# Performance work log

Hardware: AMD Instinct MI355X
Metric: run time of the kernel (lower is better)

The kernel has to match this reference:

```python
import jax, jax.numpy as jnp
import numpy as np

N_S, N_G, D, K = 30000, 3000, 128, 16
SIGMA = 2.5
BOX = 60.0  # Angstrom box for random coordinates


def setup_inputs() -> dict:
    key = jax.random.key(0)
    ks = jax.random.split(key, 10)
    s = 1.0 / np.sqrt(D)
    return {
        'xs': jax.random.normal(ks[0], (N_S, D), jnp.float32),
        'xg': jax.random.normal(ks[1], (N_G, D), jnp.float32),
        'pos_s': jax.random.uniform(ks[2], (N_S, 3), jnp.float32) * BOX,
        'pos_g': jax.random.uniform(ks[3], (N_G, 3), jnp.float32) * BOX,
        'W_s_pre': jax.random.normal(ks[4], (D, D), jnp.float32) * s,
        'W_g_pre': jax.random.normal(ks[5], (D, D), jnp.float32) * s,
        'W_gs': jax.random.normal(ks[6], (D, D), jnp.float32) * s,
        'W_sg': jax.random.normal(ks[7], (D, D), jnp.float32) * s,
        'W_s_post': jax.random.normal(ks[8], (2 * D, D), jnp.float32) * s,
        'W_g_post': jax.random.normal(ks[9], (2 * D, D), jnp.float32) * s,
        'k': K,
    }


def reference(xs, xg, pos_s, pos_g, W_s_pre, W_g_pre, W_gs, W_sg, W_s_post, W_g_post, k):
    n_s, d = xs.shape
    # ---- compute_bipartite_graphs: knn of each graph node over surface nodes ----
    # squared pairwise distances via gemm form: (N_G, N_S)
    d2 = ((pos_g ** 2).sum(-1)[:, None] + (pos_s ** 2).sum(-1)[None, :]
          - 2.0 * pos_g @ pos_s.T)
    neg_d2, idx = jax.lax.top_k(-d2, k)          # idx: (N_G, K) surface neighbors
    w = jnp.exp(neg_d2 / (2.0 * SIGMA ** 2))     # RBF edge weight exp(-d^2/(2*sigma^2))
    # ---- pre blocks ----
    hs = xs @ W_s_pre                             # (N_S, D)
    hg = xg @ W_g_pre                             # (N_G, D)
    # ---- bp_gs block: graph -> surface weighted edge-conv (scatter-add) ----
    msg_gs = (hg @ W_gs)[:, None, :] * w[:, :, None]          # (N_G, K, D)
    xs_out = jnp.zeros((n_s, d), hs.dtype).at[idx.reshape(-1)].add(
        msg_gs.reshape(-1, d))
    # ---- bp_sg block: surface -> graph weighted edge-conv (gather-sum) ----
    xg_out = ((hs @ W_sg)[idx] * w[:, :, None]).sum(axis=1)   # (N_G, D)
    # ---- post blocks: combine pre features with message output ----
    xs_new = jax.nn.relu(jnp.concatenate([hs, xs_out], axis=-1) @ W_s_post)
    xg_new = jax.nn.relu(jnp.concatenate([hg, xg_out], axis=-1) @ W_g_post)
    return xs_new, xg_new
```

## Files before the change

kernel.cpp:

```cpp
#include <hip/hip_runtime.h>
#include <stdint.h>

#define N_S 30000
#define N_G 3000
#define DD  128
#define KK  16
#define NE  (N_G * KK)
#define NC  16
#define CELLS (NC * NC * NC)
#define CH  3.75f
#define CAP 16
#define SURV 384
#define ECAP 32
#define EOVF_CAP 8192

#define FILL_BLOCKS 118
#define PACK_BLOCKS 384
#define NBS16 1875
#define NBG16 188
#define PRE_TILES (NBS16 + NBG16)
#define GROUPS 1032
#define GRID3 (GROUPS * 5)
#define NBS 469
#define NBG 47
#define NTILE (NBS + NBG)

typedef unsigned long long ull;
#define INF_KEY 0x7F7FFFFF7FFFFFFFull

using v8s = __attribute__((ext_vector_type(8))) short;
using v4f = __attribute__((ext_vector_type(4))) float;

__device__ __forceinline__ float bf2f(unsigned short u) {
    union { unsigned int i; float f; } v; v.i = ((unsigned int)u) << 16; return v.f;
}
__device__ __forceinline__ unsigned short f2bf(float f) {
    union { float f; unsigned int i; } v; v.f = f;
    unsigned int x = v.i;
    return (unsigned short)((x + 0x7fffu + ((x >> 16) & 1u)) >> 16);
}
__device__ __forceinline__ float ldIn(const void* p, int i, int bf) {
    return bf ? bf2f(((const unsigned short*)p)[i]) : ((const float*)p)[i];
}
__device__ __forceinline__ void stOut(void* p, int i, float v, int bf) {
    if (bf) ((unsigned short*)p)[i] = f2bf(v);
    else    ((float*)p)[i] = v;
}
__device__ __forceinline__ int cellOf(float x) {
    int c = (int)(x * (1.0f / CH));
    if (c < 0) c = 0; if (c > NC - 1) c = NC - 1;
    return c;
}
__device__ __forceinline__ float dist2(float gx, float gy, float gz, float4 cd) {
    const float dx = gx - cd.x, dy = gy - cd.y, dz = gz - cd.z;
    return fmaf(dx, dx, fmaf(dy, dy, dz * dz));
}
__device__ __forceinline__ ull packKey(float d2, int sid) {
    return ((ull)__float_as_uint(d2) << 32) | (unsigned)sid;
}

__device__ __forceinline__ int detectFlag(const void* pos_g) {
    const unsigned int* w = (const unsigned int*)pos_g;
    int votes = 0;
#pragma unroll
    for (int i = 0; i < 16; ++i) {
        const unsigned int b = (w[i] >> 8) & 0xFFu;
        votes += (b >= 0x3Eu && b <= 0x42u) ? 1 : 0;
    }
    return votes >= 8;
}

__device__ __forceinline__ void emitEdge(int g, ull key, int rank,
                                         int* __restrict__ idx_out,
                                         float* __restrict__ w_out,
                                         int* __restrict__ scnt,
                                         int2* __restrict__ edge,
                                         int4* __restrict__ eovf,
                                         int* __restrict__ neovf)
{
    const int sid = (int)(unsigned)key;
    const float d2 = __uint_as_float((unsigned)(key >> 32));
    const float wv = expf(-d2 * (1.0f / 12.5f));
    idx_out[g * KK + rank] = sid;
    w_out[g * KK + rank] = wv;
    const int c = atomicAdd(&scnt[sid], 1);
    if (c < ECAP) {
        edge[(size_t)sid * ECAP + c] = make_int2(g, __float_as_int(wv));
    } else {
        const int o = atomicAdd(neovf, 1);
        if (o < EOVF_CAP) eovf[o] = make_int4(sid, g, __float_as_int(wv), 0);
    }
}

__device__ __forceinline__ void ins16(ull key, ull bk[KK]) {
    if (key >= bk[KK - 1]) return;
    ull c = key;
#pragma unroll
    for (int j = 0; j < KK; ++j) {
        const bool less = c < bk[j];
        const ull nk = less ? c : bk[j];
        const ull ok = less ? bk[j] : c;
        bk[j] = nk; c = ok;
    }
}

template<int R>
__device__ __forceinline__ float regionM2f(float gx, float gy, float gz,
                                           int cx, int cy, int cz)
{
    float m = 1e30f;
    if (cx - R > 0)      m = fminf(m, gx - (float)(cx - R) * CH);
    if (cx + R < NC - 1) m = fminf(m, (float)(cx + R + 1) * CH - gx);
    if (cy - R > 0)      m = fminf(m, gy - (float)(cy - R) * CH);
    if (cy + R < NC - 1) m = fminf(m, (float)(cy + R + 1) * CH - gy);
    if (cz - R > 0)      m = fminf(m, gz - (float)(cz - R) * CH);
    if (cz + R < NC - 1) m = fminf(m, (float)(cz + R + 1) * CH - gz);
    m = fmaxf(m, 0.f);
    return (m < 1e29f) ? m * m * (1.0f - 1e-5f) : 1e30f;
}

template<int R>
__device__ int scanR(int t, float gx, float gy, float gz,
                     int cx, int cy, int cz, float m2eff,
                     const int* __restrict__ ccnt,
                     const float4* __restrict__ scell,
                     const float4* __restrict__ ovf, int novf,
                     ull* __restrict__ skey)
{
    const int S = 2 * R + 1;
    const int S3 = S * S * S;
    int total = 0;

    for (int b0 = 0; b0 < 2 * S3; b0 += 64) {
        const int pt = b0 + t;
        int cnt = 0, base = 0;
        if (pt < 2 * S3) {
            const int cell = pt >> 1, h = pt & 1;
            const int dx = cell / (S * S) - R;
            const int dy = (cell / S) % S - R;
            const int dz = cell % S - R;
            const int X = cx + dx, Y = cy + dy, Z = cz + dz;
            if (X >= 0 && X < NC && Y >= 0 && Y < NC && Z >= 0 && Z < NC) {
                const int cid = (X * NC + Y) * NC + Z;
                int c = ccnt[cid]; if (c > CAP) c = CAP;
                const int lo = h * 8;
                const int hi = (c < lo + 8) ? c : (lo + 8);
                cnt = (hi > lo) ? (hi - lo) : 0;
                base = cid * CAP + lo;
            }
        }
        ull kv[8]; int okm = 0;
#pragma unroll
        for (int i = 0; i < 8; ++i) {
            kv[i] = 0;
            if (i < cnt) {
                const float4 cd = scell[base + i];
                const float d2 = dist2(gx, gy, gz, cd);
                if (d2 < m2eff) { okm |= (1 << i); kv[i] = packKey(d2, __float_as_int(cd.w)); }
            }
        }
        int myc = __popc(okm);
        int incl = myc;
        for (int d = 1; d < 64; d <<= 1) {
            int v = __shfl_up(incl, d);
            if (t >= d) incl += v;
        }
        int pos = total + (incl - myc);
        total += __shfl(incl, 63);
#pragma unroll
        for (int i = 0; i < 8; ++i) {
            if (okm & (1 << i)) {
                if (pos < SURV) skey[pos] = kv[i];
                ++pos;
            }
        }
        if (total > SURV) return total;
    }

    for (int i0 = 0; i0 < novf; i0 += 64) {
        const int i = i0 + t;
        bool act = (i < novf);
        ull key = 0;
        if (act) {
            const float4 cd = ovf[i];
            const float d2 = dist2(gx, gy, gz, cd);
            act = (d2 < m2eff);
            if (act) key = packKey(d2, __float_as_int(cd.w));
        }
        const ull b = __ballot(act);
        const int p2 = total + (int)__popcll(b & ((1ull << t) - 1ull));
        if (act && p2 < SURV) skey[p2] = key;
        total += (int)__popcll(b);
    }
    return total;
}

template<int NV>
__device__ void rankEmit(int t, int n, const ull* __restrict__ skey, int g,
                         int* __restrict__ idx_out, float* __restrict__ w_out,
                         int* __restrict__ scnt, int2* __restrict__ edge,
                         int4* __restrict__ eovf, int* __restrict__ neovf)
{
    asm volatile("s_waitcnt lgkmcnt(0)" ::: "memory");
    ull ki[NV]; int rk[NV]; int nv = 0;
    for (int i = t; i < n && nv < NV; i += 64) { ki[nv] = skey[i]; rk[nv] = 0; ++nv; }
    for (int j = 0; j < n; ++j) {
        const ull kj = skey[j];
#pragma unroll
        for (int q = 0; q < NV; ++q)
            if (q < nv) rk[q] += (kj < ki[q]) ? 1 : 0;
    }
#pragma unroll
    for (int q = 0; q < NV; ++q)
        if (q < nv && rk[q] < KK)
            emitEdge(g, ki[q], rk[q], idx_out, w_out, scnt, edge, eovf, neovf);
}

__device__ void knn_node(int g, int bf, const void* pos_g,
                         const int* __restrict__ ccnt,
                         const float4* __restrict__ scell,
                         const float4* __restrict__ ovf, int novf,
                         int* __restrict__ idx_out, float* __restrict__ w_out,
                         int* __restrict__ scnt, int2* __restrict__ edge,
                         int4* __restrict__ eovf, int* __restrict__ neovf,
                         unsigned short* __restrict__ map16,
                         int* __restrict__ s_base, int* __restrict__ s_pref,
                         ull* __restrict__ g_key)
{
    const int t = threadIdx.x;

    const float gx = ldIn(pos_g, 3 * g + 0, bf);
    const float gy = ldIn(pos_g, 3 * g + 1, bf);
    const float gz = ldIn(pos_g, 3 * g + 2, bf);
    const int cx = cellOf(gx), cy = cellOf(gy), cz = cellOf(gz);

    ull bk[KK];
#pragma unroll
    for (int j = 0; j < KK; ++j) bk[j] = INF_KEY;

    for (int i = t; i < novf; i += 64) {
        const float4 cd = ovf[i];
        ins16(packKey(dist2(gx, gy, gz, cd), __float_as_int(cd.w)), bk);
    }

    float gk15 = 3.0e38f;
    for (int R = 1; R <= NC; ++R) {
        const int S = 2 * R + 1;
        const int Scells = S * S * S;
        for (int cb = 0; cb < Scells; cb += 64) {
            const int ci = cb + t;
            int cnt = 0, base = 0;
            if (ci < Scells) {
                const int dz = ci % S - R;
                const int dy = (ci / S) % S - R;
                const int dx = ci / (S * S) - R;
                int ax = dx < 0 ? -dx : dx, ay = dy < 0 ? -dy : dy, az = dz < 0 ? -dz : dz;
                int cheb = ax > ay ? ax : ay; if (az > cheb) cheb = az;
                const bool want = (R == 1) ? true : (cheb == R);
                const int X = cx + dx, Y = cy + dy, Z = cz + dz;
                if (want && X >= 0 && X < NC && Y >= 0 && Y < NC && Z >= 0 && Z < NC) {
                    float m2c = 0.f;
                    {
                        const float lo = (float)X * CH, hi = lo + CH;
                        const float d = (gx < lo) ? (lo - gx) : ((gx > hi) ? (gx - hi) : 0.f);
                        m2c = fmaf(d, d, m2c);
                    }
                    {
                        const float lo = (float)Y * CH, hi = lo + CH;
                        const float d = (gy < lo) ? (lo - gy) : ((gy > hi) ? (gy - hi) : 0.f);
                        m2c = fmaf(d, d, m2c);
                    }
                    {
                        const float lo = (float)Z * CH, hi = lo + CH;
                        const float d = (gz < lo) ? (lo - gz) : ((gz > hi) ? (gz - hi) : 0.f);
                        m2c = fmaf(d, d, m2c);
                    }
                    if (m2c <= gk15 * (1.0f + 1e-5f) + 1e-30f) {
                        const int cid = (X * NC + Y) * NC + Z;
                        int c = ccnt[cid]; if (c > CAP) c = CAP;
                        cnt = c; base = cid * CAP;
                    }
                }
            }
            int incl = cnt;
            for (int d = 1; d < 64; d <<= 1) {
                int v = __shfl_up(incl, d);
                if (t >= d) incl += v;
            }
            const int total = __shfl(incl, 63);
            const int pref = incl - cnt;
            s_base[t] = base; s_pref[t] = pref;
            for (int i = 0; i < cnt; ++i) map16[pref + i] = (unsigned short)t;
            __syncthreads();
            for (int pos = t; pos < total; pos += 64) {
                const int slot = map16[pos];
                const float4 cd = scell[s_base[slot] + (pos - s_pref[slot])];
                ins16(packKey(dist2(gx, gy, gz, cd), __float_as_int(cd.w)), bk);
            }
            __syncthreads();
        }
        for (int p = 0; p < KK; ++p) {
            ull key = bk[0];
            for (int d = 1; d < 64; d <<= 1) {
                const ull ok = __shfl_xor(key, d);
                if (ok < key) key = ok;
            }
            if (t == 0) g_key[p] = key;
            if (bk[0] == key) {
#pragma unroll
                for (int j = 0; j < KK - 1; ++j) bk[j] = bk[j + 1];
                bk[KK - 1] = INF_KEY;
            }
        }
        __syncthreads();
        gk15 = __uint_as_float((unsigned)(g_key[KK - 1] >> 32));
        if (t == 0) {
#pragma unroll
            for (int j = 0; j < KK; ++j) bk[j] = g_key[j];
        } else {
#pragma unroll
            for (int j = 0; j < KK; ++j) bk[j] = INF_KEY;
        }
        __syncthreads();
        float m = 1e30f;
        if (cx - R > 0)      m = fminf(m, gx - (float)(cx - R) * CH);
        if (cx + R < NC - 1) m = fminf(m, (float)(cx + R + 1) * CH - gx);
        if (cy - R > 0)      m = fminf(m, gy - (float)(cy - R) * CH);
        if (cy + R < NC - 1) m = fminf(m, (float)(cy + R + 1) * CH - gy);
        if (cz - R > 0)      m = fminf(m, gz - (float)(cz - R) * CH);
        if (cz + R < NC - 1) m = fminf(m, (float)(cz + R + 1) * CH - gz);
        m = fmaxf(m, 0.f);
        if (gk15 < m * m * (1.0f - 1e-5f)) break;
    }

    if (t == 0)
        for (int p = 0; p < KK; ++p)
            emitEdge(g, g_key[p], p, idx_out, w_out, scnt, edge, eovf, neovf);
}

__device__ __forceinline__ v8s loadA_bf16(const unsigned short* p) {
    return *(const v8s*)p;
}
__device__ __forceinline__ v8s loadA_f32v(const float* f) {
    const float4 a = *(const float4*)f;
    const float4 b = *(const float4*)(f + 4);
    v8s r;
    r[0] = (short)f2bf(a.x); r[1] = (short)f2bf(a.y);
    r[2] = (short)f2bf(a.z); r[3] = (short)f2bf(a.w);
    r[4] = (short)f2bf(b.x); r[5] = (short)f2bf(b.y);
    r[6] = (short)f2bf(b.z); r[7] = (short)f2bf(b.w);
    return r;
}
__device__ __forceinline__ v8s loadA_raw(const void* A, size_t off, int bf) {
    if (bf) return loadA_bf16((const unsigned short*)A + off);
    return loadA_f32v((const float*)A + off);
}

__device__ void pre_tile16(int task, int lane, int bf, const void* xs, const void* xg,
                           const unsigned short* __restrict__ wpk_ps,
                           const unsigned short* __restrict__ wpk_pg,
                           unsigned short* __restrict__ hsb,
                           unsigned short* __restrict__ hgb)
{
    const void* A; const unsigned short* wpk; unsigned short* outp; int M, m0;
    const bool is_s = (task < NBS16);
    if (is_s) { A = xs; wpk = wpk_ps; outp = hsb; M = N_S; m0 = task * 16; }
    else      { A = xg; wpk = wpk_pg; outp = hgb; M = N_G; m0 = (task - NBS16) * 16; }

    const int q = lane >> 4, lm = lane & 15;
    const int mrow = m0 + lm;
    const bool valid = (mrow < M);

    v4f acc[8];
#pragma unroll
    for (int t = 0; t < 8; ++t) acc[t] = {0.f, 0.f, 0.f, 0.f};
    for (int ks = 0; ks < 4; ++ks) {
        v8s a = {0,0,0,0,0,0,0,0};
        if (valid) a = loadA_raw(A, (size_t)mrow * 128 + ks * 32 + q * 8, bf);
        const unsigned short* wb = wpk + (size_t)(ks * 4 + q) * 128 * 8;
#pragma unroll
        for (int t = 0; t < 8; ++t) {
            const v8s bfr = *(const v8s*)(wb + (t * 16 + lm) * 8);
            acc[t] = __builtin_amdgcn_mfma_f32_16x16x32_bf16(a, bfr, acc[t], 0, 0, 0);
        }
    }
#pragma unroll
    for (int t = 0; t < 8; ++t)
#pragma unroll
        for (int r = 0; r < 4; ++r) {
            const int row = m0 + q * 4 + r;
            if (row < M) outp[(size_t)row * 128 + t * 16 + lm] = f2bf(acc[t][r]);
        }
}

__device__ void post_tile(int task, int bf,
                          const unsigned short* __restrict__ hsb,
                          const unsigned short* __restrict__ hgb,
                          const int* __restrict__ scnt,
                          const int2* __restrict__ edge,
                          const int4* __restrict__ eovf, int nov2,
                          const int* __restrict__ idx, const float* __restrict__ w,
                          const unsigned short* __restrict__ wpk_cs,
                          const unsigned short* __restrict__ wpk_cg,
                          void* out)
{
    const unsigned short* A1; const unsigned short* wpk;
    int M, m0, ooff;
    const bool is_s = (task < NBS);
    if (is_s) { A1 = hsb; wpk = wpk_cs; M = N_S; m0 = task * 64; ooff = 0; }
    else      { A1 = hgb; wpk = wpk_cg; M = N_G; m0 = (task - NBS) * 64; ooff = N_S * DD; }

    const int wave = threadIdx.x >> 6, lane = threadIdx.x & 63;
    const int q = lane >> 4, lm = lane & 15;
    const int mb = m0 + wave * 16;
    const int mrow = mb + lm;
    const bool valid = (mrow < M);

    v8s a2[4];
    if (valid) {
        float f[4][8];
#pragma unroll
        for (int si = 0; si < 4; ++si)
#pragma unroll
            for (int j = 0; j < 8; ++j) f[si][j] = 0.f;
        if (is_s) {
            const int c = scnt[mrow];
            const int cc = (c < ECAP) ? c : ECAP;
            for (int e = 0; e < cc; ++e) {
                const int2 ed = edge[(size_t)mrow * ECAP + e];
                const float we = __int_as_float(ed.y);
                const unsigned short* hrow = hgb + (size_t)ed.x * 128 + q * 8;
#pragma unroll
                for (int si = 0; si < 4; ++si) {
                    const v8s hv = *(const v8s*)(hrow + si * 32);
#pragma unroll
                    for (int j = 0; j < 8; ++j)
                        f[si][j] += we * bf2f((unsigned short)hv[j]);
                }
            }
            if (c > ECAP) {
                for (int e = 0; e < nov2; ++e) {
                    const int4 ov = eovf[e];
                    if (ov.x == mrow) {
                        const float we = __int_as_float(ov.z);
                        const unsigned short* hrow = hgb + (size_t)ov.y * 128 + q * 8;
#pragma unroll
                        for (int si = 0; si < 4; ++si) {
                            const v8s hv = *(const v8s*)(hrow + si * 32);
#pragma unroll
                            for (int j = 0; j < 8; ++j)
                                f[si][j] += we * bf2f((unsigned short)hv[j]);
                        }
                    }
                }
            }
        } else {
            for (int e = 0; e < KK; ++e) {
                const int gi = idx[mrow * KK + e];
                const float we = w[mrow * KK + e];
                const unsigned short* hrow = hsb + (size_t)gi * 128 + q * 8;
#pragma unroll
                for (int si = 0; si < 4; ++si) {
                    const v8s hv = *(const v8s*)(hrow + si * 32);
#pragma unroll
                    for (int j = 0; j < 8; ++j)
                        f[si][j] += we * bf2f((unsigned short)hv[j]);
                }
            }
        }
#pragma unroll
        for (int si = 0; si < 4; ++si) {
            v8s r;
#pragma unroll
            for (int j = 0; j < 8; ++j) r[j] = (short)f2bf(f[si][j]);
            a2[si] = r;
        }
    } else {
#pragma unroll
        for (int si = 0; si < 4; ++si) a2[si] = (v8s){0,0,0,0,0,0,0,0};
    }

    v4f acc[8];
#pragma unroll
    for (int t = 0; t < 8; ++t) acc[t] = {0.f, 0.f, 0.f, 0.f};
#pragma unroll
    for (int ks = 0; ks < 8; ++ks) {
        const int kk = ks * 32 + q * 8;
        v8s a;
        if (ks < 4) {
            a = (v8s){0,0,0,0,0,0,0,0};
            if (valid) a = loadA_bf16(A1 + (size_t)mrow * 128 + kk);
        } else {
            a = a2[ks - 4];
        }
        const unsigned short* wb = wpk + (size_t)(ks * 4 + q) * 128 * 8;
#pragma unroll
        for (int t = 0; t < 8; ++t) {
            const v8s bfr = *(const v8s*)(wb + (t * 16 + lm) * 8);
            acc[t] = __builtin_amdgcn_mfma_f32_16x16x32_bf16(a, bfr, acc[t], 0, 0, 0);
        }
    }
#pragma unroll
    for (int t = 0; t < 8; ++t)
#pragma unroll
        for (int r = 0; r < 4; ++r) {
            const int row = mb + q * 4 + r;
            if (row < M) {
                float v = acc[t][r];
                if (v < 0.f) v = 0.f;
                stOut(out, ooff + row * DD + t * 16 + lm, v, bf);
            }
        }
}

__global__ __launch_bounds__(256) void fill_pack_kernel(
    const void* pos_s, const void* pos_g,
    const void* Wsp, const void* Wgp, const void* Wgs, const void* Wsg,
    const void* Wspost, const void* Wgpost,
    int* __restrict__ ccnt, float4* __restrict__ scell,
    float4* __restrict__ ovf, int* __restrict__ novf,
    unsigned short* __restrict__ wpk_ps, unsigned short* __restrict__ wpk_pg,
    unsigned short* __restrict__ wpk_cs, unsigned short* __restrict__ wpk_cg)
{
    const int bf = detectFlag(pos_g);
    const int bid = blockIdx.x, tid = threadIdx.x;
    if (bid < FILL_BLOCKS) {
        const int p = bid * 256 + tid;
        if (p < N_S) {
            const float x = ldIn(pos_s, 3 * p + 0, bf);
            const float y = ldIn(pos_s, 3 * p + 1, bf);
            const float z = ldIn(pos_s, 3 * p + 2, bf);
            const int cid = (cellOf(x) * NC + cellOf(y)) * NC + cellOf(z);
            const int slot = atomicAdd(&ccnt[cid], 1);
            const float4 pt = make_float4(x, y, z, __int_as_float(p));
            if (slot < CAP) scell[cid * CAP + slot] = pt;
            else            ovf[atomicAdd(novf, 1)] = pt;
        }
        return;
    }
    __shared__ float rows[256];
    const int rt = bid - FILL_BLOCKS;
    const int half = tid >> 7, j = tid & 127;
    const int task = rt * 2 + half;
    float v; unsigned short* dst; int k;
    if (task < 128) { k = task; v = ldIn(Wsp, k * DD + j, bf); dst = wpk_ps; }
    else if (task < 256) { k = task - 128; v = ldIn(Wgp, k * DD + j, bf); dst = wpk_pg; }
    else {
        const int which_g = (task >= 512);
        const int r = which_g ? (task - 512) : (task - 256);
        const void* W1 = which_g ? Wsg : Wgs;
        const void* Wp = which_g ? Wgpost : Wspost;
        dst = which_g ? wpk_cg : wpk_cs;
        k = r;
        if (r < 128) v = ldIn(Wp, r * DD + j, bf);
        else {
            rows[half * 128 + j] = ldIn(W1, (r - 128) * DD + j, bf);
            __syncthreads();
            float acc = 0.f;
            for (int m = 0; m < DD; ++m)
                acc += rows[half * 128 + m] * ldIn(Wp, (DD + m) * DD + j, bf);
            v = acc;
        }
    }
    const int ks = k >> 5, q = (k >> 3) & 3, i = k & 7;
    dst[((ks * 4 + q) * 128 + j) * 8 + i] = f2bf(v);
}

__global__ __launch_bounds__(64) void knn_pre_kernel(
    const void* xs, const void* xg, const void* pos_g,
    const int* __restrict__ ccnt, const float4* __restrict__ scell,
    const float4* __restrict__ ovf, const int* __restrict__ novf,
    int* __restrict__ idx, float* __restrict__ w,
    int* __restrict__ scnt, int2* __restrict__ edge,
    int4* __restrict__ eovf, int* __restrict__ neovf,
    const unsigned short* __restrict__ wpk_ps,
    const unsigned short* __restrict__ wpk_pg,
    unsigned short* __restrict__ hsb, unsigned short* __restrict__ hgb)
{
    const int bf = detectFlag(pos_g);
    const int bid = blockIdx.x;
    const int group = bid / 5, off = bid - group * 5;
    if (off < 3) {
        const int g = group * 3 + off;
        if (g >= N_G) return;
        __shared__ ull skey[SURV];
        const int t = threadIdx.x;
        const int nov = *novf;

        const float gx = ldIn(pos_g, 3 * g + 0, bf);
        const float gy = ldIn(pos_g, 3 * g + 1, bf);
        const float gz = ldIn(pos_g, 3 * g + 2, bf);
        const int cx = cellOf(gx), cy = cellOf(gy), cz = cellOf(gz);

        bool done = false;
        int total = scanR<1>(t, gx, gy, gz, cx, cy, cz,
                             regionM2f<1>(gx, gy, gz, cx, cy, cz),
                             ccnt, scell, ovf, nov, skey);
        if (total >= KK && total <= SURV) {
            rankEmit<3>(t, total, skey, g, idx, w, scnt, edge, eovf, neovf);
            done = true;
        } else if (total < KK) {
            total = scanR<2>(t, gx, gy, gz, cx, cy, cz,
                             regionM2f<2>(gx, gy, gz, cx, cy, cz),
                             ccnt, scell, ovf, nov, skey);
            if (total >= KK && total <= SURV) {
                rankEmit<6>(t, total, skey, g, idx, w, scnt, edge, eovf, neovf);
                done = true;
            }
        }
        if (!done) {
            __shared__ unsigned short map16[64 * CAP];
            __shared__ int s_base[64];
            __shared__ int s_pref[64];
            __shared__ ull g_key[KK];
            __syncthreads();
            knn_node(g, bf, pos_g, ccnt, scell, ovf, nov, idx, w,
                     scnt, edge, eovf, neovf, map16, s_base, s_pref, g_key);
        }
    } else {
        const int task = group * 2 + (off - 3);
        if (task >= PRE_TILES) return;
        pre_tile16(task, threadIdx.x, bf, xs, xg, wpk_ps, wpk_pg, hsb, hgb);
    }
}

__global__ __launch_bounds__(256) void mfma_post_kernel(
    const void* pos_g,
    const unsigned short* __restrict__ hsb, const unsigned short* __restrict__ hgb,
    const int* __restrict__ scnt, const int2* __restrict__ edge,
    const int4* __restrict__ eovf, const int* __restrict__ neovf,
    const int* __restrict__ idx, const float* __restrict__ w,
    const unsigned short* __restrict__ wpk_cs, const unsigned short* __restrict__ wpk_cg,
    void* out)
{
    const int bf = detectFlag(pos_g);
    int nov2 = *neovf; if (nov2 > EOVF_CAP) nov2 = EOVF_CAP;
    post_tile(blockIdx.x, bf, hsb, hgb, scnt, edge, eovf, nov2,
              idx, w, wpk_cs, wpk_cg, out);
}

extern "C" void kernel_launch(void* const* d_in, const int* in_sizes, int n_in,
                              void* d_out, int out_size, void* d_ws, size_t ws_size,
                              hipStream_t stream)
{
    const void* xs       = d_in[0];
    const void* xg       = d_in[1];
    const void* pos_s    = d_in[2];
    const void* pos_g    = d_in[3];
    const void* W_s_pre  = d_in[4];
    const void* W_g_pre  = d_in[5];
    const void* W_gs     = d_in[6];
    const void* W_sg     = d_in[7];
    const void* W_s_post = d_in[8];
    const void* W_g_post = d_in[9];
    (void)in_sizes; (void)n_in; (void)out_size; (void)ws_size;

    char* ws = (char*)d_ws;
    size_t off_b = 0;
    auto alloc = [&](size_t bytes) -> void* {
        void* p = ws + off_b;
        off_b = (off_b + bytes + 255) & ~((size_t)255);
        return p;
    };
    unsigned short* hsb    = (unsigned short*)alloc((size_t)N_S * DD * 2);
    unsigned short* hgb    = (unsigned short*)alloc((size_t)N_G * DD * 2);
    unsigned short* wpk_ps = (unsigned short*)alloc((size_t)DD * DD * 2);
    unsigned short* wpk_pg = (unsigned short*)alloc((size_t)DD * DD * 2);
    unsigned short* wpk_cs = (unsigned short*)alloc((size_t)2 * DD * DD * 2);
    unsigned short* wpk_cg = (unsigned short*)alloc((size_t)2 * DD * DD * 2);
    int*            idx    = (int*)   alloc((size_t)NE * 4);
    float*          w      = (float*) alloc((size_t)NE * 4);
    int*            ibase  = (int*)   alloc((size_t)(CELLS + 1 + N_S + 1) * 4);
    int*            ccnt   = ibase;
    int*            novf   = ibase + CELLS;
    int*            scnt   = ibase + CELLS + 1;
    int*            neovf  = ibase + CELLS + 1 + N_S;
    float4*         scell  = (float4*)alloc((size_t)CELLS * CAP * 16);
    float4*         ovf    = (float4*)alloc((size_t)N_S * 16);
    int2*           edge   = (int2*)  alloc((size_t)N_S * ECAP * 8);
    int4*           eovf   = (int4*)  alloc((size_t)EOVF_CAP * 16);

    hipMemsetAsync(ibase, 0, (size_t)(CELLS + 1 + N_S + 1) * 4, stream);

    fill_pack_kernel<<<FILL_BLOCKS + PACK_BLOCKS, 256, 0, stream>>>(
        pos_s, pos_g, W_s_pre, W_g_pre, W_gs, W_sg, W_s_post, W_g_post,
        ccnt, scell, ovf, novf, wpk_ps, wpk_pg, wpk_cs, wpk_cg);

    knn_pre_kernel<<<GRID3, 64, 0, stream>>>(
        xs, xg, pos_g, ccnt, scell, ovf, novf, idx, w,
        scnt, edge, eovf, neovf, wpk_ps, wpk_pg, hsb, hgb);

    mfma_post_kernel<<<NTILE, 256, 0, stream>>>(
        pos_g, hsb, hgb, scnt, edge, eovf, neovf, idx, w,
        wpk_cs, wpk_cg, d_out);
}
```

Baseline: 172.4 us.

## Use persistent wave-level work queue for knn/pre tasks with brute-force fallback

Replaces the one-block-per-task grid of 64-thread blocks with persistent 256-thread blocks in which each wave pulls knn or pre-GEMM tasks from a global atomic counter. The aim is to cut launch and scheduling overhead and to balance uneven knn work. The expanding-shell knn fallback is replaced by a brute-force scan over all surface points for the rare nodes whose neighbourhood overflows. The scan path picks rankEmit<3> or rankEmit<6> based on the candidate count. The queue adds atomic contention, and the brute-force fallback can be expensive when it is hit.

```diff
diff --git a/kernel.cpp b/kernel.cpp
--- a/kernel.cpp
+++ b/kernel.cpp
@@ -19,8 +19,8 @@
 #define NBS16 1875
 #define NBG16 188
 #define PRE_TILES (NBS16 + NBG16)
-#define GROUPS 1032
-#define GRID3 (GROUPS * 5)
+#define TASKS 5160
+#define QBLOCKS 768
 #define NBS 469
 #define NBG 47
 #define NTILE (NBS + NBG)
@@ -216,126 +216,78 @@
             emitEdge(g, ki[q], rk[q], idx_out, w_out, scnt, edge, eovf, neovf);
 }
 
-__device__ void knn_node(int g, int bf, const void* pos_g,
+__attribute__((noinline))
+__device__ void knn_brute(int g, int t, int bf,
+                          const void* pos_g, const void* pos_s,
+                          int* __restrict__ idx_out, float* __restrict__ w_out,
+                          int* __restrict__ scnt, int2* __restrict__ edge,
+                          int4* __restrict__ eovf, int* __restrict__ neovf)
+{
+    const float gx = ldIn(pos_g, 3 * g + 0, bf);
+    const float gy = ldIn(pos_g, 3 * g + 1, bf);
+    const float gz = ldIn(pos_g, 3 * g + 2, bf);
+
+    ull bk[KK];
+#pragma unroll
+    for (int j = 0; j < KK; ++j) bk[j] = INF_KEY;
+
+    for (int i = t; i < N_S; i += 64) {
+        const float dx = gx - ldIn(pos_s, 3 * i + 0, bf);
+        const float dy = gy - ldIn(pos_s, 3 * i + 1, bf);
+        const float dz = gz - ldIn(pos_s, 3 * i + 2, bf);
+        const float d2 = fmaf(dx, dx, fmaf(dy, dy, dz * dz));
+        ins16(packKey(d2, i), bk);
+    }
+
+    ull myKey = INF_KEY;
+    for (int p = 0; p < KK; ++p) {
+        ull key = bk[0];
+        for (int d = 1; d < 64; d <<= 1) {
+            const ull ok = __shfl_xor(key, d);
+            if (ok < key) key = ok;
+        }
+        if (t == p) myKey = key;
+        if (bk[0] == key) {
+#pragma unroll
+            for (int j = 0; j < KK - 1; ++j) bk[j] = bk[j + 1];
+            bk[KK - 1] = INF_KEY;
+        }
+    }
+    if (t < KK)
+        emitEdge(g, myKey, t, idx_out, w_out, scnt, edge, eovf, neovf);
+}
+
+__device__ void knn_task(int g, int t, int bf,
+                         const void* pos_g, const void* pos_s,
                          const int* __restrict__ ccnt,
                          const float4* __restrict__ scell,
                          const float4* __restrict__ ovf, int novf,
-                         int* __restrict__ idx_out, float* __restrict__ w_out,
+                         int* __restrict__ idx, float* __restrict__ w,
                          int* __restrict__ scnt, int2* __restrict__ edge,
                          int4* __restrict__ eovf, int* __restrict__ neovf,
-                         unsigned short* __restrict__ map16,
-                         int* __restrict__ s_base, int* __restrict__ s_pref,
-                         ull* __restrict__ g_key)
-{
-    const int t = threadIdx.x;
-
+                         ull* __restrict__ skey)
+{
     const float gx = ldIn(pos_g, 3 * g + 0, bf);
     const float gy = ldIn(pos_g, 3 * g + 1, bf);
     const float gz = ldIn(pos_g, 3 * g + 2, bf);
     const int cx = cellOf(gx), cy = cellOf(gy), cz = cellOf(gz);
 
-    ull bk[KK];
-#pragma unroll
-    for (int j = 0; j < KK; ++j) bk[j] = INF_KEY;
-
-    for (int i = t; i < novf; i += 64) {
-        const float4 cd = ovf[i];
-        ins16(packKey(dist2(gx, gy, gz, cd), __float_as_int(cd.w)), bk);
-    }
-
-    float gk15 = 3.0e38f;
-    for (int R = 1; R <= NC; ++R) {
-        const int S = 2 * R + 1;
-        const int Scells = S * S * S;
-        for (int cb = 0; cb < Scells; cb += 64) {
-            const int ci = cb + t;
-            int cnt = 0, base = 0;
-            if (ci < Scells) {
-                const int dz = ci % S - R;
-                const int dy = (ci / S) % S - R;
-                const int dx = ci / (S * S) - R;
-                int ax = dx < 0 ? -dx : dx, ay = dy < 0 ? -dy : dy, az = dz < 0 ? -dz : dz;
-                int cheb = ax > ay ? ax : ay; if (az > cheb) cheb = az;
-                const bool want = (R == 1) ? true : (cheb == R);
-                const int X = cx + dx, Y = cy + dy, Z = cz + dz;
-                if (want && X >= 0 && X < NC && Y >= 0 && Y < NC && Z >= 0 && Z < NC) {
-                    float m2c = 0.f;
-                    {
-                        const float lo = (float)X * CH, hi = lo + CH;
-                        const float d = (gx < lo) ? (lo - gx) : ((gx > hi) ? (gx - hi) : 0.f);
-                        m2c = fmaf(d, d, m2c);
-                    }
-                    {
-                        const float lo = (float)Y * CH, hi = lo + CH;
-                        const float d = (gy < lo) ? (lo - gy) : ((gy > hi) ? (gy - hi) : 0.f);
-                        m2c = fmaf(d, d, m2c);
-                    }
-                    {
-                        const float lo = (float)Z * CH, hi = lo + CH;
-                        const float d = (gz < lo) ? (lo - gz) : ((gz > hi) ? (gz - hi) : 0.f);
-                        m2c = fmaf(d, d, m2c);
-                    }
-                    if (m2c <= gk15 * (1.0f + 1e-5f) + 1e-30f) {
-                        const int cid = (X * NC + Y) * NC + Z;
-                        int c = ccnt[cid]; if (c > CAP) c = CAP;
-                        cnt = c; base = cid * CAP;
-                    }
-                }
-            }
-            int incl = cnt;
-            for (int d = 1; d < 64; d <<= 1) {
-                int v = __shfl_up(incl, d);
-                if (t >= d) incl += v;
-            }
-            const int total = __shfl(incl, 63);
-            const int pref = incl - cnt;
-            s_base[t] = base; s_pref[t] = pref;
-            for (int i = 0; i < cnt; ++i) map16[pref + i] = (unsigned short)t;
-            __syncthreads();
-            for (int pos = t; pos < total; pos += 64) {
-                const int slot = map16[pos];
-                const float4 cd = scell[s_base[slot] + (pos - s_pref[slot])];
-                ins16(packKey(dist2(gx, gy, gz, cd), __float_as_int(cd.w)), bk);
-            }
-            __syncthreads();
-        }
-        for (int p = 0; p < KK; ++p) {
-            ull key = bk[0];
-            for (int d = 1; d < 64; d <<= 1) {
-                const ull ok = __shfl_xor(key, d);
-                if (ok < key) key = ok;
-            }
-            if (t == 0) g_key[p] = key;
-            if (bk[0] == key) {
-#pragma unroll
-                for (int j = 0; j < KK - 1; ++j) bk[j] = bk[j + 1];
-                bk[KK - 1] = INF_KEY;
-            }
-        }
-        __syncthreads();
-        gk15 = __uint_as_float((unsigned)(g_key[KK - 1] >> 32));
-        if (t == 0) {
-#pragma unroll
-            for (int j = 0; j < KK; ++j) bk[j] = g_key[j];
-        } else {
-#pragma unroll
-            for (int j = 0; j < KK; ++j) bk[j] = INF_KEY;
-        }
-        __syncthreads();
-        float m = 1e30f;
-        if (cx - R > 0)      m = fminf(m, gx - (float)(cx - R) * CH);
-        if (cx + R < NC - 1) m = fminf(m, (float)(cx + R + 1) * CH - gx);
-        if (cy - R > 0)      m = fminf(m, gy - (float)(cy - R) * CH);
-        if (cy + R < NC - 1) m = fminf(m, (float)(cy + R + 1) * CH - gy);
-        if (cz - R > 0)      m = fminf(m, gz - (float)(cz - R) * CH);
-        if (cz + R < NC - 1) m = fminf(m, (float)(cz + R + 1) * CH - gz);
-        m = fmaxf(m, 0.f);
-        if (gk15 < m * m * (1.0f - 1e-5f)) break;
-    }
-
-    if (t == 0)
-        for (int p = 0; p < KK; ++p)
-            emitEdge(g, g_key[p], p, idx_out, w_out, scnt, edge, eovf, neovf);
+    int total = scanR<1>(t, gx, gy, gz, cx, cy, cz,
+                         regionM2f<1>(gx, gy, gz, cx, cy, cz),
+                         ccnt, scell, ovf, novf, skey);
+    if (total < KK)
+        total = scanR<2>(t, gx, gy, gz, cx, cy, cz,
+                         regionM2f<2>(gx, gy, gz, cx, cy, cz),
+                         ccnt, scell, ovf, novf, skey);
+
+    if (total >= KK && total <= SURV) {
+        if (total <= 192)
+            rankEmit<3>(t, total, skey, g, idx, w, scnt, edge, eovf, neovf);
+        else
+            rankEmit<6>(t, total, skey, g, idx, w, scnt, edge, eovf, neovf);
+    } else {
+        knn_brute(g, t, bf, pos_g, pos_s, idx, w, scnt, edge, eovf, neovf);
+    }
 }
 
 __device__ __forceinline__ v8s loadA_bf16(const unsigned short* p) {
@@ -566,61 +518,39 @@
     dst[((ks * 4 + q) * 128 + j) * 8 + i] = f2bf(v);
 }
 
-__global__ __launch_bounds__(64) void knn_pre_kernel(
-    const void* xs, const void* xg, const void* pos_g,
+__global__ __launch_bounds__(256) void knn_pre_kernel(
+    const void* xs, const void* xg, const void* pos_s, const void* pos_g,
     const int* __restrict__ ccnt, const float4* __restrict__ scell,
     const float4* __restrict__ ovf, const int* __restrict__ novf,
     int* __restrict__ idx, float* __restrict__ w,
     int* __restrict__ scnt, int2* __restrict__ edge,
     int4* __restrict__ eovf, int* __restrict__ neovf,
+    int* __restrict__ qctr,
     const unsigned short* __restrict__ wpk_ps,
     const unsigned short* __restrict__ wpk_pg,
     unsigned short* __restrict__ hsb, unsigned short* __restrict__ hgb)
 {
+    __shared__ ull skey[4][SURV];
     const int bf = detectFlag(pos_g);
-    const int bid = blockIdx.x;
-    const int group = bid / 5, off = bid - group * 5;
-    if (off < 3) {
-        const int g = group * 3 + off;
-        if (g >= N_G) return;
-        __shared__ ull skey[SURV];
-        const int t = threadIdx.x;
-        const int nov = *novf;
-
-        const float gx = ldIn(pos_g, 3 * g + 0, bf);
-        const float gy = ldIn(pos_g, 3 * g + 1, bf);
-        const float gz = ldIn(pos_g, 3 * g + 2, bf);
-        const int cx = cellOf(gx), cy = cellOf(gy), cz = cellOf(gz);
-
-        bool done = false;
-        int total = scanR<1>(t, gx, gy, gz, cx, cy, cz,
-                             regionM2f<1>(gx, gy, gz, cx, cy, cz),
-                             ccnt, scell, ovf, nov, skey);
-        if (total >= KK && total <= SURV) {
-            rankEmit<3>(t, total, skey, g, idx, w, scnt, edge, eovf, neovf);
-            done = true;
-        } else if (total < KK) {
-            total = scanR<2>(t, gx, gy, gz, cx, cy, cz,
-                             regionM2f<2>(gx, gy, gz, cx, cy, cz),
-                             ccnt, scell, ovf, nov, skey);
-            if (total >= KK && total <= SURV) {
-                rankEmit<6>(t, total, skey, g, idx, w, scnt, edge, eovf, neovf);
-                done = true;
-            }
-        }
-        if (!done) {
-            __shared__ unsigned short map16[64 * CAP];
-            __shared__ int s_base[64];
-            __shared__ int s_pref[64];
-            __shared__ ull g_key[KK];
-            __syncthreads();
-            knn_node(g, bf, pos_g, ccnt, scell, ovf, nov, idx, w,
-                     scnt, edge, eovf, neovf, map16, s_base, s_pref, g_key);
-        }
-    } else {
-        const int task = group * 2 + (off - 3);
-        if (task >= PRE_TILES) return;
-        pre_tile16(task, threadIdx.x, bf, xs, xg, wpk_ps, wpk_pg, hsb, hgb);
+    const int wv = threadIdx.x >> 6, lane = threadIdx.x & 63;
+    const int nov = *novf;
+
+    for (;;) {
+        int t0 = 0;
+        if (lane == 0) t0 = atomicAdd(qctr, 1);
+        t0 = __shfl(t0, 0);
+        if (t0 >= TASKS) break;
+        const int grp = t0 / 5, off = t0 - grp * 5;
+        if (off < 3) {
+            const int g = grp * 3 + off;
+            if (g < N_G)
+                knn_task(g, lane, bf, pos_g, pos_s, ccnt, scell, ovf, nov,
+                         idx, w, scnt, edge, eovf, neovf, skey[wv]);
+        } else {
+            const int task = grp * 2 + (off - 3);
+            if (task < PRE_TILES)
+                pre_tile16(task, lane, bf, xs, xg, wpk_ps, wpk_pg, hsb, hgb);
+        }
     }
 }
 
@@ -670,25 +600,26 @@
     unsigned short* wpk_cg = (unsigned short*)alloc((size_t)2 * DD * DD * 2);
     int*            idx    = (int*)   alloc((size_t)NE * 4);
     float*          w      = (float*) alloc((size_t)NE * 4);
-    int*            ibase  = (int*)   alloc((size_t)(CELLS + 1 + N_S + 1) * 4);
+    int*            ibase  = (int*)   alloc((size_t)(CELLS + 1 + N_S + 2) * 4);
     int*            ccnt   = ibase;
     int*            novf   = ibase + CELLS;
     int*            scnt   = ibase + CELLS + 1;
     int*            neovf  = ibase + CELLS + 1 + N_S;
+    int*            qctr   = ibase + CELLS + 1 + N_S + 1;
     float4*         scell  = (float4*)alloc((size_t)CELLS * CAP * 16);
     float4*         ovf    = (float4*)alloc((size_t)N_S * 16);
     int2*           edge   = (int2*)  alloc((size_t)N_S * ECAP * 8);
     int4*           eovf   = (int4*)  alloc((size_t)EOVF_CAP * 16);
 
-    hipMemsetAsync(ibase, 0, (size_t)(CELLS + 1 + N_S + 1) * 4, stream);
+    hipMemsetAsync(ibase, 0, (size_t)(CELLS + 1 + N_S + 2) * 4, stream);
 
     fill_pack_kernel<<<FILL_BLOCKS + PACK_BLOCKS, 256, 0, stream>>>(
         pos_s, pos_g, W_s_pre, W_g_pre, W_gs, W_sg, W_s_post, W_g_post,
         ccnt, scell, ovf, novf, wpk_ps, wpk_pg, wpk_cs, wpk_cg);
 
-    knn_pre_kernel<<<GRID3, 64, 0, stream>>>(
-        xs, xg, pos_g, ccnt, scell, ovf, novf, idx, w,
-        scnt, edge, eovf, neovf, wpk_ps, wpk_pg, hsb, hgb);
+    knn_pre_kernel<<<QBLOCKS, 256, 0, stream>>>(
+        xs, xg, pos_s, pos_g, ccnt, scell, ovf, novf, idx, w,
+        scnt, edge, eovf, neovf, qctr, wpk_ps, wpk_pg, hsb, hgb);
 
     mfma_post_kernel<<<NTILE, 256, 0, stream>>>(
         pos_g, hsb, hgb, scnt, edge, eovf, neovf, idx, w,
```

Result: slower. 248.4 us (+44.1%).
